# Optimization experiments

Hardware: AMD Instinct MI355X
Metric: run time of the kernel (lower is better)

Reference implementation:

```python
import jax, jax.numpy as jnp
import numpy as np

NUM_GRAPHS = 512
BN_EPS = 1e-5

def _lin(k, fin, fout):
    kw, kb = jax.random.split(k)
    s = 1.0 / np.sqrt(fin)
    return (jax.random.uniform(kw, (fin, fout), jnp.float32, -s, s),
            jax.random.uniform(kb, (fout,), jnp.float32, -s, s))

def setup_inputs() -> dict:
    key = jax.random.key(0)
    ks = jax.random.split(key, 16)
    N, E, F, C, H, O = 50000, 800000, 128, 256, 512, 768
    x = jax.random.normal(ks[0], (N, F), jnp.float32)
    edge_index = jax.random.randint(ks[1], (2, E), 0, N, jnp.int64)
    batch = jnp.sort(jax.random.randint(ks[2], (N,), 0, NUM_GRAPHS, jnp.int64))
    d = {"x": x, "edge_index": edge_index, "batch": batch}
    d["w1a"], d["b1a"] = _lin(ks[3], F, C)
    d["g1"], d["be1"] = jnp.ones((C,), jnp.float32), jnp.zeros((C,), jnp.float32)
    d["w1b"], d["b1b"] = _lin(ks[4], C, C)
    d["w2a"], d["b2a"] = _lin(ks[5], C, C)
    d["g2"], d["be2"] = jnp.ones((C,), jnp.float32), jnp.zeros((C,), jnp.float32)
    d["w2b"], d["b2b"] = _lin(ks[6], C, C)
    d["w3a"], d["b3a"] = _lin(ks[7], C, C)
    d["g3"], d["be3"] = jnp.ones((C,), jnp.float32), jnp.zeros((C,), jnp.float32)
    d["w3b"], d["b3b"] = _lin(ks[8], C, C)
    d["wh1"], d["bh1"] = _lin(ks[9], C, H)
    d["wh2"], d["bh2"] = _lin(ks[10], H, O)
    return d

def _bn(z, g, b):
    mu = jnp.mean(z, axis=0)
    var = jnp.mean((z - mu) ** 2, axis=0)  # biased var, torch BN training mode
    return (z - mu) * jax.lax.rsqrt(var + BN_EPS) * g + b

def _gin(x, edge_index, wa, ba, g, be, wb, bb, tanh_out):
    src, dst = edge_index[0], edge_index[1]
    agg = jax.ops.segment_sum(x[src], dst, num_segments=x.shape[0])
    h = x + agg  # eps = 0
    z = jax.nn.relu(_bn(h @ wa + ba, g, be))
    z = z @ wb + bb
    return jnp.tanh(z) if tanh_out else z

def reference(x, edge_index, batch,
              w1a, b1a, g1, be1, w1b, b1b,
              w2a, b2a, g2, be2, w2b, b2b,
              w3a, b3a, g3, be3, w3b, b3b,
              wh1, bh1, wh2, bh2):
    h = jax.nn.relu(_gin(x, edge_index, w1a, b1a, g1, be1, w1b, b1b, False))
    h = jax.nn.relu(_gin(h, edge_index, w2a, b2a, g2, be2, w2b, b2b, True))
    h = _gin(h, edge_index, w3a, b3a, g3, be3, w3b, b3b, True)
    # global mean pool over graphs
    sums = jax.ops.segment_sum(h, batch, num_segments=NUM_GRAPHS)
    cnt = jax.ops.segment_sum(jnp.ones((h.shape[0],), h.dtype), batch, num_segments=NUM_GRAPHS)
    pooled = sums / jnp.maximum(cnt, 1.0)[:, None]
    z = jax.nn.relu(pooled @ wh1 + bh1)
    return z @ wh2 + bh2
```

## Files before the change

kernel.cpp:

```cpp
#include <hip/hip_runtime.h>


typedef __attribute__((ext_vector_type(8))) short short8;
typedef __attribute__((ext_vector_type(4))) float f32x4;
typedef __attribute__((ext_vector_type(4))) unsigned short us4;
typedef __attribute__((ext_vector_type(8))) unsigned short us8;

__device__ __forceinline__ unsigned short f2bf(float f) {
  unsigned int b = __float_as_uint(f);
  unsigned int r = 0x7FFFu + ((b >> 16) & 1u);
  return (unsigned short)((b + r) >> 16);
}
__device__ __forceinline__ float bf2f(unsigned short u) {
  return __uint_as_float(((unsigned int)u) << 16);
}

__device__ __forceinline__ int sw8(int row) {
  return (row & 7) ^ ((row >> 3) & 7);
}

typedef const __attribute__((address_space(1))) unsigned int* gas1;
typedef __attribute__((address_space(3))) unsigned int* las3;
__device__ __forceinline__ void gload16(const void* g, void* l) {
  __builtin_amdgcn_global_load_lds((gas1)g, (las3)l, 16, 0, 0);
}

__device__ __forceinline__ size_t swz8_idx(int row, int k, int K) {
  int g = k >> 3;
  return (size_t)row * K + ((g >> 3) << 6) + ((((g & 7) ^ sw8(row)) << 3)) + (k & 7);
}

__global__ void k_histbounds(const int* __restrict__ ei, int* __restrict__ deg, int E,
                             int eb, const int* __restrict__ batch,
                             int* __restrict__ gs, int* __restrict__ ge, int N) {
  int b = blockIdx.x;
  if (b < eb) {
    int e = b * 256 + threadIdx.x;
    if (e < E) atomicAdd(&deg[ei[E + e]], 1);
  } else {
    int i = (b - eb) * 256 + threadIdx.x;
    if (i < N) {
      int bb = batch[i];
      if (i == 0 || batch[i - 1] != bb) gs[bb] = i;
      if (i == N - 1 || batch[i + 1] != bb) ge[bb] = i + 1;
    }
  }
}

__global__ __launch_bounds__(1024) void k_scan1(const int* __restrict__ deg,
                                                int* __restrict__ partial,
                                                int* __restrict__ bsum, int N) {
  __shared__ int sd[1024];
  int tid = threadIdx.x;
  int i = blockIdx.x * 1024 + tid;
  int v = (i < N) ? deg[i] : 0;
  sd[tid] = v;
  __syncthreads();
  for (int off = 1; off < 1024; off <<= 1) {
    int t = (tid >= off) ? sd[tid - off] : 0;
    __syncthreads();
    sd[tid] += t;
    __syncthreads();
  }
  if (i < N) partial[i] = sd[tid];
  if (tid == 1023) bsum[blockIdx.x] = sd[1023];
}

__global__ void k_scan2(int* __restrict__ bsum, int nb) {
  int l = threadIdx.x;
  int orig = (l < nb) ? bsum[l] : 0;
  int v = orig;
  for (int off = 1; off < 64; off <<= 1) {
    int t = __shfl_up(v, off);
    if (l >= off) v += t;
  }
  if (l < nb) bsum[l] = v - orig;
}

__global__ void k_scan3(const int* __restrict__ deg, const int* __restrict__ partial,
                        const int* __restrict__ bsum, int* __restrict__ rowptr,
                        int* __restrict__ cursor, int N) {
  int i = blockIdx.x * 256 + threadIdx.x;
  if (i >= N) return;
  int incl = partial[i] + bsum[i >> 10];
  rowptr[i + 1] = incl;
  cursor[i] = incl - deg[i];
  if (i == 0) rowptr[0] = 0;
}

__global__ void k_fill(const int* __restrict__ ei, int* __restrict__ cursor,
                       int* __restrict__ adj, int E) {
  int e = blockIdx.x * 256 + threadIdx.x;
  if (e >= E) return;
  int s = ei[e];
  int d = ei[E + e];
  int pos = atomicAdd(&cursor[d], 1);
  adj[pos] = s;
}

__global__ void k_xbf(const float* __restrict__ X, unsigned short* __restrict__ Xb,
                      int total) {
  int t = blockIdx.x * 256 + threadIdx.x;
  if (t * 8 >= total) return;
  const float4 v0 = *(const float4*)(X + t * 8);
  const float4 v1 = *(const float4*)(X + t * 8 + 4);
  us8 o;
  o[0] = f2bf(v0.x); o[1] = f2bf(v0.y); o[2] = f2bf(v0.z); o[3] = f2bf(v0.w);
  o[4] = f2bf(v1.x); o[5] = f2bf(v1.y); o[6] = f2bf(v1.z); o[7] = f2bf(v1.w);
  *(us8*)(Xb + t * 8) = o;
}

__global__ void k_prep_all(const float* __restrict__ w1a, const float* __restrict__ w1b,
                           const float* __restrict__ w2a, const float* __restrict__ w2b,
                           const float* __restrict__ w3a, const float* __restrict__ w3b,
                           const float* __restrict__ wh1, const float* __restrict__ wh2,
                           unsigned short* __restrict__ Hi, unsigned short* __restrict__ Lo) {
  int idx = blockIdx.x * 256 + threadIdx.x;
  const float* W; int K, Nout, lo_;
  if (idx < 32768)       { W = w1a; K = 128; Nout = 256; lo_ = 0; }
  else if (idx < 98304)  { W = w1b; K = 256; Nout = 256; lo_ = 32768; }
  else if (idx < 163840) { W = w2a; K = 256; Nout = 256; lo_ = 98304; }
  else if (idx < 229376) { W = w2b; K = 256; Nout = 256; lo_ = 163840; }
  else if (idx < 294912) { W = w3a; K = 256; Nout = 256; lo_ = 229376; }
  else if (idx < 360448) { W = w3b; K = 256; Nout = 256; lo_ = 294912; }
  else if (idx < 491520) { W = wh1; K = 256; Nout = 512; lo_ = 360448; }
  else                   { W = wh2; K = 512; Nout = 768; lo_ = 491520; }
  int li = idx - lo_;
  int n = li % Nout, k = li / Nout;
  float w = W[k * Nout + n];
  unsigned short h = f2bf(w);
  size_t oi = (size_t)lo_ + swz8_idx(n, k, K);
  Hi[oi] = h;
  Lo[oi] = f2bf(w - bf2f(h));
}

template <int C>
__global__ __launch_bounds__(256) void k_agg(const unsigned short* __restrict__ Xb,
                                             unsigned short* __restrict__ Hb,
                                             const int* __restrict__ rowptr,
                                             const int* __restrict__ adj, int N,
                                             float* __restrict__ statsZ) {
  if (blockIdx.x == 0) {
    statsZ[threadIdx.x] = 0.f;
    statsZ[256 + threadIdx.x] = 0.f;
  }
  int node = blockIdx.x * 4 + (threadIdx.x >> 6);
  if (node >= N) return;
  int lane = threadIdx.x & 63;
  int e0 = rowptr[node], e1 = rowptr[node + 1];
  if constexpr (C == 256) {
    us4 ov = *(const us4*)(Xb + (size_t)node * C + lane * 4);
    float a0 = bf2f(ov[0]), a1 = bf2f(ov[1]), a2 = bf2f(ov[2]), a3 = bf2f(ov[3]);
    int e = e0;
    for (; e + 4 <= e1; e += 4) {
      int s0 = adj[e], s1 = adj[e + 1], s2 = adj[e + 2], s3 = adj[e + 3];
      us4 v0 = *(const us4*)(Xb + (size_t)s0 * C + lane * 4);
      us4 v1 = *(const us4*)(Xb + (size_t)s1 * C + lane * 4);
      us4 v2 = *(const us4*)(Xb + (size_t)s2 * C + lane * 4);
      us4 v3 = *(const us4*)(Xb + (size_t)s3 * C + lane * 4);
      a0 += (bf2f(v0[0]) + bf2f(v1[0])) + (bf2f(v2[0]) + bf2f(v3[0]));
      a1 += (bf2f(v0[1]) + bf2f(v1[1])) + (bf2f(v2[1]) + bf2f(v3[1]));
      a2 += (bf2f(v0[2]) + bf2f(v1[2])) + (bf2f(v2[2]) + bf2f(v3[2]));
      a3 += (bf2f(v0[3]) + bf2f(v1[3])) + (bf2f(v2[3]) + bf2f(v3[3]));
    }
    for (; e < e1; ++e) {
      us4 v = *(const us4*)(Xb + (size_t)adj[e] * C + lane * 4);
      a0 += bf2f(v[0]); a1 += bf2f(v[1]); a2 += bf2f(v[2]); a3 += bf2f(v[3]);
    }
    us4 hv;
    hv[0] = f2bf(a0); hv[1] = f2bf(a1); hv[2] = f2bf(a2); hv[3] = f2bf(a3);
    size_t oi = (size_t)node * 256 + ((lane >> 4) << 6) +
                ((((lane >> 1) & 7) ^ sw8(node)) << 3) + ((lane & 1) << 2);
    *(us4*)(Hb + oi) = hv;
  } else {
    ushort2 ov = *(const ushort2*)(Xb + (size_t)node * C + lane * 2);
    float a0 = bf2f(ov.x), a1 = bf2f(ov.y);
    int e = e0;
    for (; e + 4 <= e1; e += 4) {
      int s0 = adj[e], s1 = adj[e + 1], s2 = adj[e + 2], s3 = adj[e + 3];
      ushort2 v0 = *(const ushort2*)(Xb + (size_t)s0 * C + lane * 2);
      ushort2 v1 = *(const ushort2*)(Xb + (size_t)s1 * C + lane * 2);
      ushort2 v2 = *(const ushort2*)(Xb + (size_t)s2 * C + lane * 2);
      ushort2 v3 = *(const ushort2*)(Xb + (size_t)s3 * C + lane * 2);
      a0 += (bf2f(v0.x) + bf2f(v1.x)) + (bf2f(v2.x) + bf2f(v3.x));
      a1 += (bf2f(v0.y) + bf2f(v1.y)) + (bf2f(v2.y) + bf2f(v3.y));
    }
    for (; e < e1; ++e) {
      ushort2 v = *(const ushort2*)(Xb + (size_t)adj[e] * C + lane * 2);
      a0 += bf2f(v.x); a1 += bf2f(v.y);
    }
    ushort2 hv = {f2bf(a0), f2bf(a1)};
    size_t oi = (size_t)node * 128 + ((lane >> 5) << 6) +
                ((((lane >> 2) & 7) ^ sw8(node)) << 3) + ((lane & 3) << 1);
    *(ushort2*)(Hb + oi) = hv;
  }
}

template <int EPI, bool STATS, bool OSPLIT, bool XSWZ, int ASRC, bool FULL, bool OBF16>
__global__ __launch_bounds__(256) void k_gemm(
    const unsigned short* __restrict__ AHb, const unsigned short* __restrict__ ALo,
    const unsigned short* __restrict__ Zb,
    int M, int K, int Nld, int mb, int per,
    const unsigned short* __restrict__ WHi, const unsigned short* __restrict__ WLo,
    const float* __restrict__ bias,
    const float* __restrict__ statsIn, const float* __restrict__ gvec,
    const float* __restrict__ bevec,
    float* __restrict__ Out, unsigned short* __restrict__ OutB,
    unsigned short* __restrict__ OHi, unsigned short* __restrict__ OLo,
    float* __restrict__ statsOut) {
  __shared__ unsigned short aHi[4096], bHi[8192];
  __shared__ unsigned short aLo[FULL ? 4096 : 64], bLo[FULL ? 8192 : 64];
  __shared__ float sBNsc[ASRC == 2 ? 256 : 1], sBNsh[ASRC == 2 ? 256 : 1];
  int bx, by;
  if constexpr (XSWZ) {
    int xcd = blockIdx.x & 7, slot = blockIdx.x >> 3;
    bx = xcd * per + (slot >> 1);
    by = slot & 1;
    if (bx >= mb) return;
  } else {
    bx = blockIdx.x;
    by = blockIdx.y;
  }
  const int tid = threadIdx.x;
  const int lane = tid & 63, w = tid >> 6;
  const int wm = w >> 1, wn = w & 1;
  const int m0 = bx * 64, n0 = by * 128;

  if constexpr (ASRC == 2) {
    float mu = statsIn[tid] / (float)M;
    float var = statsIn[256 + tid] / (float)M - mu * mu;
    float sc = gvec[tid] * rsqrtf(var + 1e-5f);
    sBNsc[tid] = sc;
    sBNsh[tid] = bevec[tid] - mu * sc;
    __syncthreads();
  }

  f32x4 zero = {0.f, 0.f, 0.f, 0.f};
  f32x4 acc[2][4];
#pragma unroll
  for (int i = 0; i < 2; ++i)
#pragma unroll
    for (int j = 0; j < 4; ++j) acc[i][j] = zero;

  const int l8 = lane >> 3;
  const int s8 = lane & 7;

  us8 arg[2], brg[4];
  const unsigned short* aptr[2];
  const unsigned short* bptr[4];
  if constexpr (!FULL) {
    const unsigned short* asrc = (ASRC == 2) ? Zb : AHb;
#pragma unroll
    for (int p = 0; p < 2; ++p) {
      int row = (p << 5) + (tid >> 3);
      int ra = m0 + row; if (ra >= M) ra = M - 1;
      aptr[p] = asrc + (size_t)ra * K + (tid & 7) * 8;
      arg[p] = *(const us8*)(aptr[p]);
    }
#pragma unroll
    for (int q = 0; q < 4; ++q) {
      int row = (q << 5) + (tid >> 3);
      bptr[q] = WHi + (size_t)(n0 + row) * K + (tid & 7) * 8;
      brg[q] = *(const us8*)(bptr[q]);
    }
  }

  for (int kb = 0; kb < K; kb += 64) {
    if constexpr (!FULL) {
      if constexpr (ASRC == 2) {
#pragma unroll
        for (int p = 0; p < 2; ++p) {
          int row = (p << 5) + (tid >> 3), gq = tid & 7;
          us8 hv;
#pragma unroll
          for (int jj = 0; jj < 8; ++jj) {
            int kc = kb + gq * 8 + jj;
            float o = fmaxf(bf2f(arg[p][jj]) * sBNsc[kc] + sBNsh[kc], 0.f);
            hv[jj] = f2bf(o);
          }
          int bo = row * 128 + ((gq ^ sw8(row)) << 4);
          *(us8*)((char*)aHi + bo) = hv;
        }
      } else {
#pragma unroll
        for (int p = 0; p < 2; ++p) {
          int row = (p << 5) + (tid >> 3);
          int bo = row * 128 + ((tid & 7) << 4);
          *(us8*)((char*)aHi + bo) = arg[p];
        }
      }
#pragma unroll
      for (int q = 0; q < 4; ++q) {
        int row = (q << 5) + (tid >> 3);
        int bo = row * 128 + ((tid & 7) << 4);
        *(us8*)((char*)bHi + bo) = brg[q];
      }
      __syncthreads();
      if (kb + 64 < K) {
#pragma unroll
        for (int p = 0; p < 2; ++p) arg[p] = *(const us8*)(aptr[p] + kb + 64);
#pragma unroll
        for (int q = 0; q < 4; ++q) brg[q] = *(const us8*)(bptr[q] + kb + 64);
      }
    } else {
      __syncthreads();
#pragma unroll
      for (int q = 0; q < 2; ++q) {
        int row = (w << 4) + (q << 3) + l8;
        int ra = m0 + row; if (ra >= M) ra = M - 1;
        size_t ga = (size_t)ra * K + kb + s8 * 8;
        unsigned boA = (w << 11) + (q << 10);
        gload16(AHb + ga, (char*)aHi + boA);
        gload16(ALo + ga, (char*)aLo + boA);
      }
#pragma unroll
      for (int q = 0; q < 4; ++q) {
        int row = (w << 5) + (q << 3) + l8;
        size_t gb = (size_t)(n0 + row) * K + kb + s8 * 8;
        unsigned bo2 = (w << 12) + (q << 10);
        gload16(WHi + gb, (char*)bHi + bo2);
        gload16(WLo + gb, (char*)bLo + bo2);
      }
      __syncthreads();
    }

    const int j = lane >> 4;
#pragma unroll
    for (int kk = 0; kk < 2; ++kk) {
      int g = (kk << 2) + j;
      short8 bh[4], bl[4];
#pragma unroll
      for (int ni = 0; ni < 4; ++ni) {
        int r = wn * 64 + ni * 16 + (lane & 15);
        int bo = r * 128 + ((g ^ sw8(r)) << 4);
        bh[ni] = *(const short8*)((const char*)bHi + bo);
        if constexpr (FULL) bl[ni] = *(const short8*)((const char*)bLo + bo);
      }
#pragma unroll
      for (int mi = 0; mi < 2; ++mi) {
        int r = wm * 32 + mi * 16 + (lane & 15);
        int bo = r * 128 + ((g ^ sw8(r)) << 4);
        short8 ah = *(const short8*)((const char*)aHi + bo);
#pragma unroll
        for (int ni = 0; ni < 4; ++ni) {
          acc[mi][ni] = __builtin_amdgcn_mfma_f32_16x16x32_bf16(ah, bh[ni], acc[mi][ni], 0, 0, 0);
          if constexpr (FULL) {
            short8 al = *(const short8*)((const char*)aLo + bo);
            acc[mi][ni] = __builtin_amdgcn_mfma_f32_16x16x32_bf16(ah, bl[ni], acc[mi][ni], 0, 0, 0);
            acc[mi][ni] = __builtin_amdgcn_mfma_f32_16x16x32_bf16(al, bh[ni], acc[mi][ni], 0, 0, 0);
          }
        }
      }
    }
    if constexpr (!FULL) __syncthreads();
  }

#pragma unroll
  for (int ni = 0; ni < 4; ++ni) {
    int col = n0 + wn * 64 + ni * 16 + (lane & 15);
    float bc = bias[col];
    float s = 0.f, q = 0.f;
#pragma unroll
    for (int mi = 0; mi < 2; ++mi) {
      int rbase = m0 + wm * 32 + mi * 16 + (lane >> 4) * 4;
#pragma unroll
      for (int r = 0; r < 4; ++r) {
        int row = rbase + r;
        if (row < M) {
          float o = acc[mi][ni][r] + bc;
          if (STATS) { s += o; q += o * o; }
          if (OSPLIT) {
            o = fmaxf(o, 0.f);
            unsigned short h = f2bf(o);
            size_t oi = swz8_idx(row, col, Nld);
            OHi[oi] = h;
            OLo[oi] = f2bf(o - bf2f(h));
          } else {
            if (EPI == 1) o = fmaxf(o, 0.f);
            else if (EPI == 2) o = tanhf(o);
            else if (EPI == 3) o = fmaxf(tanhf(o), 0.f);
            if (OBF16) OutB[(size_t)row * Nld + col] = f2bf(o);
            else       Out[(size_t)row * Nld + col] = o;
          }
        }
      }
    }
    if (STATS) {
      s += __shfl_xor(s, 16); s += __shfl_xor(s, 32);
      q += __shfl_xor(q, 16); q += __shfl_xor(q, 32);
      if ((lane >> 4) == 0) {
        atomicAdd(&statsOut[col], s);
        atomicAdd(&statsOut[256 + col], q);
      }
    }
  }
}

__global__ __launch_bounds__(256) void k_pool(const unsigned short* __restrict__ Hb,
                                              const int* __restrict__ gs,
                                              const int* __restrict__ ge,
                                              unsigned short* __restrict__ PHi,
                                              unsigned short* __restrict__ PLo) {
  __shared__ float4 red[4][64];
  int gi = blockIdx.x;
  int s = gs[gi], e = ge[gi];
  int w = threadIdx.x >> 6, lane = threadIdx.x & 63;
  float4 acc = {0.f, 0.f, 0.f, 0.f};
  for (int r = s + w; r < e; r += 4) {
    us4 v = *(const us4*)(Hb + (size_t)r * 256 + lane * 4);
    acc.x += bf2f(v[0]); acc.y += bf2f(v[1]);
    acc.z += bf2f(v[2]); acc.w += bf2f(v[3]);
  }
  red[w][lane] = acc;
  __syncthreads();
  if (w == 0) {
    float4 a = red[0][lane], b = red[1][lane], c = red[2][lane], d = red[3][lane];
    float inv = 1.0f / fmaxf((float)(e - s), 1.0f);
    float vv[4] = {(a.x + b.x + c.x + d.x) * inv, (a.y + b.y + c.y + d.y) * inv,
                   (a.z + b.z + c.z + d.z) * inv, (a.w + b.w + c.w + d.w) * inv};
    us4 hv, lv;
#pragma unroll
    for (int j = 0; j < 4; ++j) {
      unsigned short h = f2bf(vv[j]);
      hv[j] = h;
      lv[j] = f2bf(vv[j] - bf2f(h));
    }
    size_t oi = (size_t)gi * 256 + ((lane >> 4) << 6) +
                ((((lane >> 1) & 7) ^ sw8(gi)) << 3) + ((lane & 1) << 2);
    *(us4*)(PHi + oi) = hv;
    *(us4*)(PLo + oi) = lv;
  }
}

extern "C" void kernel_launch(void* const* d_in, const int* in_sizes, int n_in,
                              void* d_out, int out_size, void* d_ws, size_t ws_size,
                              hipStream_t stream) {
  const float* x      = (const float*)d_in[0];
  const int* ei       = (const int*)d_in[1];
  const int* bat      = (const int*)d_in[2];
  const float* w1a = (const float*)d_in[3];  const float* b1a = (const float*)d_in[4];
  const float* g1  = (const float*)d_in[5];  const float* be1 = (const float*)d_in[6];
  const float* w1b = (const float*)d_in[7];  const float* b1b = (const float*)d_in[8];
  const float* w2a = (const float*)d_in[9];  const float* b2a = (const float*)d_in[10];
  const float* g2  = (const float*)d_in[11]; const float* be2 = (const float*)d_in[12];
  const float* w2b = (const float*)d_in[13]; const float* b2b = (const float*)d_in[14];
  const float* w3a = (const float*)d_in[15]; const float* b3a = (const float*)d_in[16];
  const float* g3  = (const float*)d_in[17]; const float* be3 = (const float*)d_in[18];
  const float* w3b = (const float*)d_in[19]; const float* b3b = (const float*)d_in[20];
  const float* wh1 = (const float*)d_in[21]; const float* bh1 = (const float*)d_in[22];
  const float* wh2 = (const float*)d_in[23]; const float* bh2 = (const float*)d_in[24];
  float* out = (float*)d_out;

  const int N = in_sizes[0] / 128;
  const int E = in_sizes[1] / 2;
  const int G = 512;

  char* ws = (char*)d_ws;
  size_t off = 0;
  auto alloc = [&](size_t bytes) {
    void* p = ws + off;
    off = (off + bytes + 255) & ~(size_t)255;
    return p;
  };
  unsigned short* hb = (unsigned short*)alloc((size_t)N * 256 * 2);
  unsigned short* zb = (unsigned short*)alloc((size_t)N * 256 * 2);
  unsigned short* ab = (unsigned short*)alloc((size_t)N * 256 * 2);
  unsigned short* xb = (unsigned short*)alloc((size_t)N * 128 * 2);
  int* adj     = (int*)alloc((size_t)E * 4);
  int* rowptr  = (int*)alloc((size_t)(N + 1) * 4);
  int* cursor  = (int*)alloc((size_t)N * 4);
  int* deg     = (int*)alloc((size_t)N * 4);
  int* partial = (int*)alloc((size_t)N * 4);
  int* bsum    = (int*)alloc(64 * 4);
  unsigned short* wHi = (unsigned short*)alloc(884736 * 2);
  unsigned short* wLo = (unsigned short*)alloc(884736 * 2);
  float* stats = (float*)alloc(512 * 4);
  int* gs      = (int*)alloc(G * 4);
  int* ge      = (int*)alloc(G * 4);
  unsigned short* poolHi = (unsigned short*)alloc((size_t)G * 256 * 2);
  unsigned short* poolLo = (unsigned short*)alloc((size_t)G * 256 * 2);
  unsigned short* thidHi = (unsigned short*)alloc((size_t)G * 512 * 2);
  unsigned short* thidLo = (unsigned short*)alloc((size_t)G * 512 * 2);

  const int o1a = 0, o1b = 32768, o2a = 98304, o2b = 163840, o3a = 229376, o3b = 294912;
  const int oh1 = 360448, oh2 = 491520;

  hipMemsetAsync(deg, 0, (size_t)N * 4, stream);
  hipMemsetAsync(gs, 0, (size_t)G * 4, stream);
  hipMemsetAsync(ge, 0, (size_t)G * 4, stream);

  int eb = (E + 255) / 256;
  int nbN = (N + 255) / 256;
  int nb1 = (N + 1023) >> 10;
  k_histbounds<<<eb + nbN, 256, 0, stream>>>(ei, deg, E, eb, bat, gs, ge, N);
  k_scan1<<<nb1, 1024, 0, stream>>>(deg, partial, bsum, N);
  k_scan2<<<1, 64, 0, stream>>>(bsum, nb1);
  k_scan3<<<nbN, 256, 0, stream>>>(deg, partial, bsum, rowptr, cursor, N);
  k_fill<<<eb, 256, 0, stream>>>(ei, cursor, adj, E);

  k_xbf<<<(N * 128 / 8 + 255) / 256, 256, 0, stream>>>(x, xb, N * 128);
  k_prep_all<<<3456, 256, 0, stream>>>(w1a, w1b, w2a, w2b, w3a, w3b, wh1, wh2, wHi, wLo);

  int nb4 = (N + 3) / 4;
  const int mb = (N + 63) / 64;
  const int per = (mb + 7) / 8;
  dim3 gg(per * 16);

  k_agg<128><<<nb4, 256, 0, stream>>>(xb, hb, rowptr, adj, N, stats);
  k_gemm<0, true, false, true, 0, false, true><<<gg, 256, 0, stream>>>(
      hb, nullptr, nullptr, N, 128, 256, mb, per, wHi + o1a, wLo + o1a, b1a,
      nullptr, nullptr, nullptr, nullptr, zb, nullptr, nullptr, stats);
  k_gemm<1, false, false, true, 2, false, true><<<gg, 256, 0, stream>>>(
      nullptr, nullptr, zb, N, 256, 256, mb, per, wHi + o1b, wLo + o1b, b1b,
      stats, g1, be1, nullptr, ab, nullptr, nullptr, nullptr);

  k_agg<256><<<nb4, 256, 0, stream>>>(ab, hb, rowptr, adj, N, stats);
  k_gemm<0, true, false, true, 0, false, true><<<gg, 256, 0, stream>>>(
      hb, nullptr, nullptr, N, 256, 256, mb, per, wHi + o2a, wLo + o2a, b2a,
      nullptr, nullptr, nullptr, nullptr, zb, nullptr, nullptr, stats);
  k_gemm<3, false, false, true, 2, false, true><<<gg, 256, 0, stream>>>(
      nullptr, nullptr, zb, N, 256, 256, mb, per, wHi + o2b, wLo + o2b, b2b,
      stats, g2, be2, nullptr, ab, nullptr, nullptr, nullptr);

  k_agg<256><<<nb4, 256, 0, stream>>>(ab, hb, rowptr, adj, N, stats);
  k_gemm<0, true, false, true, 0, false, true><<<gg, 256, 0, stream>>>(
      hb, nullptr, nullptr, N, 256, 256, mb, per, wHi + o3a, wLo + o3a, b3a,
      nullptr, nullptr, nullptr, nullptr, zb, nullptr, nullptr, stats);
  k_gemm<2, false, false, true, 2, false, true><<<gg, 256, 0, stream>>>(
      nullptr, nullptr, zb, N, 256, 256, mb, per, wHi + o3b, wLo + o3b, b3b,
      stats, g3, be3, nullptr, ab, nullptr, nullptr, nullptr);

  k_pool<<<G, 256, 0, stream>>>(ab, gs, ge, poolHi, poolLo);
  dim3 gh1(8, 4);
  k_gemm<1, false, true, false, 0, true, false><<<gh1, 256, 0, stream>>>(
      poolHi, poolLo, nullptr, G, 256, 512, 0, 0, wHi + oh1, wLo + oh1, bh1,
      nullptr, nullptr, nullptr, nullptr, nullptr, thidHi, thidLo, nullptr);
  dim3 gh2(8, 6);
  k_gemm<0, false, false, false, 0, true, false><<<gh2, 256, 0, stream>>>(
      thidHi, thidLo, nullptr, G, 512, 768, 0, 0, wHi + oh2, wLo + oh2, bh2,
      nullptr, nullptr, nullptr, out, nullptr, nullptr, nullptr, nullptr);
}
```

Baseline: 577.3 us.

## Use persistent node GEMM keeping full weight slice in LDS, A read directly to registers

Splits the generic GEMM into a persistent node-layer kernel and a head kernel. The node-layer kernel loads its whole 128-column weight slice into LDS once, then loops over several 64-row tiles. For each tile it reads the A rows straight from global memory into MFMA fragment registers, which removes the per-K-step LDS staging and barriers for A. The aggregation output is written unswizzled to match the new row-major A reads. This trades barrier and LDS traffic for a larger LDS footprint (up to 64KB), which may lower occupancy, and for uncoalesced fragment-pattern global loads.

Result: slower. 700.1 us (+21.3%).

```diff
diff --git a/kernel.cpp b/kernel.cpp
--- a/kernel.cpp
+++ b/kernel.cpp
@@ -169,9 +169,7 @@
     }
     us4 hv;
     hv[0] = f2bf(a0); hv[1] = f2bf(a1); hv[2] = f2bf(a2); hv[3] = f2bf(a3);
-    size_t oi = (size_t)node * 256 + ((lane >> 4) << 6) +
-                ((((lane >> 1) & 7) ^ sw8(node)) << 3) + ((lane & 1) << 2);
-    *(us4*)(Hb + oi) = hv;
+    *(us4*)(Hb + (size_t)node * C + lane * 4) = hv;
   } else {
     ushort2 ov = *(const ushort2*)(Xb + (size_t)node * C + lane * 2);
     float a0 = bf2f(ov.x), a1 = bf2f(ov.y);
@@ -190,41 +188,31 @@
       a0 += bf2f(v.x); a1 += bf2f(v.y);
     }
     ushort2 hv = {f2bf(a0), f2bf(a1)};
-    size_t oi = (size_t)node * 128 + ((lane >> 5) << 6) +
-                ((((lane >> 2) & 7) ^ sw8(node)) << 3) + ((lane & 3) << 1);
-    *(ushort2*)(Hb + oi) = hv;
-  }
-}
-
-template <int EPI, bool STATS, bool OSPLIT, bool XSWZ, int ASRC, bool FULL, bool OBF16>
-__global__ __launch_bounds__(256) void k_gemm(
-    const unsigned short* __restrict__ AHb, const unsigned short* __restrict__ ALo,
-    const unsigned short* __restrict__ Zb,
-    int M, int K, int Nld, int mb, int per,
-    const unsigned short* __restrict__ WHi, const unsigned short* __restrict__ WLo,
+    *(ushort2*)(Hb + (size_t)node * C + lane * 2) = hv;
+  }
+}
+
+template <int EPI, bool STATS, int ASRC, int KT>
+__global__ __launch_bounds__(256) void k_gemmM(
+    const unsigned short* __restrict__ Ab, int M,
+    const unsigned short* __restrict__ WHi,
     const float* __restrict__ bias,
     const float* __restrict__ statsIn, const float* __restrict__ gvec,
     const float* __restrict__ bevec,
-    float* __restrict__ Out, unsigned short* __restrict__ OutB,
-    unsigned short* __restrict__ OHi, unsigned short* __restrict__ OLo,
-    float* __restrict__ statsOut) {
-  __shared__ unsigned short aHi[4096], bHi[8192];
-  __shared__ unsigned short aLo[FULL ? 4096 : 64], bLo[FULL ? 8192 : 64];
+    unsigned short* __restrict__ OutB,
+    float* __restrict__ statsOut,
+    int mb, int per) {
+  constexpr int SLOTS = KT / 8;
+  constexpr int KS = KT / 32;
+  __shared__ unsigned short bB[128 * KT];
   __shared__ float sBNsc[ASRC == 2 ? 256 : 1], sBNsh[ASRC == 2 ? 256 : 1];
-  int bx, by;
-  if constexpr (XSWZ) {
-    int xcd = blockIdx.x & 7, slot = blockIdx.x >> 3;
-    bx = xcd * per + (slot >> 1);
-    by = slot & 1;
-    if (bx >= mb) return;
-  } else {
-    bx = blockIdx.x;
-    by = blockIdx.y;
-  }
+
   const int tid = threadIdx.x;
   const int lane = tid & 63, w = tid >> 6;
   const int wm = w >> 1, wn = w & 1;
-  const int m0 = bx * 64, n0 = by * 128;
+  const int xcd = blockIdx.x & 7, slot = blockIdx.x >> 3;
+  const int by = slot & 1, bseq = slot >> 1;
+  const int n0 = by * 128;
 
   if constexpr (ASRC == 2) {
     float mu = statsIn[tid] / (float)M;
@@ -232,8 +220,126 @@
     float sc = gvec[tid] * rsqrtf(var + 1e-5f);
     sBNsc[tid] = sc;
     sBNsh[tid] = bevec[tid] - mu * sc;
-    __syncthreads();
-  }
+  }
+
+  constexpr int ROUNDS = (128 * SLOTS) / 256;
+#pragma unroll
+  for (int q = 0; q < ROUNDS; ++q) {
+    int cb = q * 256 + w * 64;
+    int c = cb + lane;
+    int row = c / SLOTS, sl = c % SLOTS;
+    size_t gb = (size_t)(n0 + row) * KT + sl * 8;
+    gload16(WHi + gb, (char*)bB + cb * 16);
+  }
+  __syncthreads();
+
+  const int fr = lane & 15;
+  const int j4 = lane >> 4;
+  const int fk = j4 * 8;
+
+  for (int i = 0;; ++i) {
+    int bxl = bseq + i * 32;
+    if (bxl >= per) break;
+    int bx = xcd * per + bxl;
+    if (bx >= mb) break;
+    int m0 = bx * 64;
+
+    us8 av[2][KS];
+#pragma unroll
+    for (int mi = 0; mi < 2; ++mi) {
+      int ra = m0 + wm * 32 + mi * 16 + fr;
+      if (ra >= M) ra = M - 1;
+      const unsigned short* ap = Ab + (size_t)ra * KT + fk;
+#pragma unroll
+      for (int ks = 0; ks < KS; ++ks) av[mi][ks] = *(const us8*)(ap + ks * 32);
+    }
+    if constexpr (ASRC == 2) {
+#pragma unroll
+      for (int mi = 0; mi < 2; ++mi)
+#pragma unroll
+        for (int ks = 0; ks < KS; ++ks) {
+#pragma unroll
+          for (int jj = 0; jj < 8; ++jj) {
+            int kc = ks * 32 + fk + jj;
+            float o = fmaxf(bf2f(av[mi][ks][jj]) * sBNsc[kc] + sBNsh[kc], 0.f);
+            av[mi][ks][jj] = f2bf(o);
+          }
+        }
+    }
+
+    f32x4 acc[2][4];
+    f32x4 zero = {0.f, 0.f, 0.f, 0.f};
+#pragma unroll
+    for (int a = 0; a < 2; ++a)
+#pragma unroll
+      for (int b = 0; b < 4; ++b) acc[a][b] = zero;
+
+#pragma unroll
+    for (int ks = 0; ks < KS; ++ks) {
+      int g = ks * 4 + j4;
+      short8 bh[4];
+#pragma unroll
+      for (int ni = 0; ni < 4; ++ni) {
+        int r = wn * 64 + ni * 16 + fr;
+        int bo = r * (KT * 2) + ((g >> 3) << 7) + (((g & 7) ^ sw8(r)) << 4);
+        bh[ni] = *(const short8*)((const char*)bB + bo);
+      }
+#pragma unroll
+      for (int mi = 0; mi < 2; ++mi)
+#pragma unroll
+        for (int ni = 0; ni < 4; ++ni)
+          acc[mi][ni] = __builtin_amdgcn_mfma_f32_16x16x32_bf16(
+              (short8)av[mi][ks], bh[ni], acc[mi][ni], 0, 0, 0);
+    }
+
+#pragma unroll
+    for (int ni = 0; ni < 4; ++ni) {
+      int col = n0 + wn * 64 + ni * 16 + fr;
+      float bc = bias[col];
+      float s = 0.f, qq = 0.f;
+#pragma unroll
+      for (int mi = 0; mi < 2; ++mi) {
+        int rbase = m0 + wm * 32 + mi * 16 + (lane >> 4) * 4;
+#pragma unroll
+        for (int r = 0; r < 4; ++r) {
+          int row = rbase + r;
+          if (row < M) {
+            float o = acc[mi][ni][r] + bc;
+            if (STATS) { s += o; qq += o * o; }
+            if (EPI == 1) o = fmaxf(o, 0.f);
+            else if (EPI == 2) o = tanhf(o);
+            else if (EPI == 3) o = fmaxf(tanhf(o), 0.f);
+            OutB[(size_t)row * 256 + col] = f2bf(o);
+          }
+        }
+      }
+      if (STATS) {
+        s += __shfl_xor(s, 16); s += __shfl_xor(s, 32);
+        qq += __shfl_xor(qq, 16); qq += __shfl_xor(qq, 32);
+        if ((lane >> 4) == 0) {
+          atomicAdd(&statsOut[col], s);
+          atomicAdd(&statsOut[256 + col], qq);
+        }
+      }
+    }
+  }
+}
+
+template <int EPI, bool OSPLIT>
+__global__ __launch_bounds__(256) void k_gemmH(
+    const unsigned short* __restrict__ AHb, const unsigned short* __restrict__ ALo,
+    int M, int K, int Nld,
+    const unsigned short* __restrict__ WHi, const unsigned short* __restrict__ WLo,
+    const float* __restrict__ bias,
+    float* __restrict__ Out,
+    unsigned short* __restrict__ OHi, unsigned short* __restrict__ OLo) {
+  __shared__ unsigned short aHi[4096], bHi[8192];
+  __shared__ unsigned short aLo[4096], bLo[8192];
+  int bx = blockIdx.x, by = blockIdx.y;
+  const int tid = threadIdx.x;
+  const int lane = tid & 63, w = tid >> 6;
+  const int wm = w >> 1, wn = w & 1;
+  const int m0 = bx * 64, n0 = by * 128;
 
   f32x4 zero = {0.f, 0.f, 0.f, 0.f};
   f32x4 acc[2][4];
@@ -245,84 +351,26 @@
   const int l8 = lane >> 3;
   const int s8 = lane & 7;
 
-  us8 arg[2], brg[4];
-  const unsigned short* aptr[2];
-  const unsigned short* bptr[4];
-  if constexpr (!FULL) {
-    const unsigned short* asrc = (ASRC == 2) ? Zb : AHb;
-#pragma unroll
-    for (int p = 0; p < 2; ++p) {
-      int row = (p << 5) + (tid >> 3);
+  for (int kb = 0; kb < K; kb += 64) {
+    __syncthreads();
+#pragma unroll
+    for (int q = 0; q < 2; ++q) {
+      int row = (w << 4) + (q << 3) + l8;
       int ra = m0 + row; if (ra >= M) ra = M - 1;
-      aptr[p] = asrc + (size_t)ra * K + (tid & 7) * 8;
-      arg[p] = *(const us8*)(aptr[p]);
+      size_t ga = (size_t)ra * K + kb + s8 * 8;
+      unsigned boA = (w << 11) + (q << 10);
+      gload16(AHb + ga, (char*)aHi + boA);
+      gload16(ALo + ga, (char*)aLo + boA);
     }
 #pragma unroll
     for (int q = 0; q < 4; ++q) {
-      int row = (q << 5) + (tid >> 3);
-      bptr[q] = WHi + (size_t)(n0 + row) * K + (tid & 7) * 8;
-      brg[q] = *(const us8*)(bptr[q]);
-    }
-  }
-
-  for (int kb = 0; kb < K; kb += 64) {
-    if constexpr (!FULL) {
-      if constexpr (ASRC == 2) {
-#pragma unroll
-        for (int p = 0; p < 2; ++p) {
-          int row = (p << 5) + (tid >> 3), gq = tid & 7;
-          us8 hv;
-#pragma unroll
-          for (int jj = 0; jj < 8; ++jj) {
-            int kc = kb + gq * 8 + jj;
-            float o = fmaxf(bf2f(arg[p][jj]) * sBNsc[kc] + sBNsh[kc], 0.f);
-            hv[jj] = f2bf(o);
-          }
-          int bo = row * 128 + ((gq ^ sw8(row)) << 4);
-          *(us8*)((char*)aHi + bo) = hv;
-        }
-      } else {
-#pragma unroll
-        for (int p = 0; p < 2; ++p) {
-          int row = (p << 5) + (tid >> 3);
-          int bo = row * 128 + ((tid & 7) << 4);
-          *(us8*)((char*)aHi + bo) = arg[p];
-        }
-      }
-#pragma unroll
-      for (int q = 0; q < 4; ++q) {
-        int row = (q << 5) + (tid >> 3);
-        int bo = row * 128 + ((tid & 7) << 4);
-        *(us8*)((char*)bHi + bo) = brg[q];
-      }
-      __syncthreads();
-      if (kb + 64 < K) {
-#pragma unroll
-        for (int p = 0; p < 2; ++p) arg[p] = *(const us8*)(aptr[p] + kb + 64);
-#pragma unroll
-        for (int q = 0; q < 4; ++q) brg[q] = *(const us8*)(bptr[q] + kb + 64);
-      }
-    } else {
-      __syncthreads();
-#pragma unroll
-      for (int q = 0; q < 2; ++q) {
-        int row = (w << 4) + (q << 3) + l8;
-        int ra = m0 + row; if (ra >= M) ra = M - 1;
-        size_t ga = (size_t)ra * K + kb + s8 * 8;
-        unsigned boA = (w << 11) + (q << 10);
-        gload16(AHb + ga, (char*)aHi + boA);
-        gload16(ALo + ga, (char*)aLo + boA);
-      }
-#pragma unroll
-      for (int q = 0; q < 4; ++q) {
-        int row = (w << 5) + (q << 3) + l8;
-        size_t gb = (size_t)(n0 + row) * K + kb + s8 * 8;
-        unsigned bo2 = (w << 12) + (q << 10);
-        gload16(WHi + gb, (char*)bHi + bo2);
-        gload16(WLo + gb, (char*)bLo + bo2);
-      }
-      __syncthreads();
-    }
+      int row = (w << 5) + (q << 3) + l8;
+      size_t gb = (size_t)(n0 + row) * K + kb + s8 * 8;
+      unsigned bo2 = (w << 12) + (q << 10);
+      gload16(WHi + gb, (char*)bHi + bo2);
+      gload16(WLo + gb, (char*)bLo + bo2);
+    }
+    __syncthreads();
 
     const int j = lane >> 4;
 #pragma unroll
@@ -334,32 +382,28 @@
         int r = wn * 64 + ni * 16 + (lane & 15);
         int bo = r * 128 + ((g ^ sw8(r)) << 4);
         bh[ni] = *(const short8*)((const char*)bHi + bo);
-        if constexpr (FULL) bl[ni] = *(const short8*)((const char*)bLo + bo);
+        bl[ni] = *(const short8*)((const char*)bLo + bo);
       }
 #pragma unroll
       for (int mi = 0; mi < 2; ++mi) {
         int r = wm * 32 + mi * 16 + (lane & 15);
         int bo = r * 128 + ((g ^ sw8(r)) << 4);
         short8 ah = *(const short8*)((const char*)aHi + bo);
+        short8 al = *(const short8*)((const char*)aLo + bo);
 #pragma unroll
         for (int ni = 0; ni < 4; ++ni) {
           acc[mi][ni] = __builtin_amdgcn_mfma_f32_16x16x32_bf16(ah, bh[ni], acc[mi][ni], 0, 0, 0);
-          if constexpr (FULL) {
-            short8 al = *(const short8*)((const char*)aLo + bo);
-            acc[mi][ni] = __builtin_amdgcn_mfma_f32_16x16x32_bf16(ah, bl[ni], acc[mi][ni], 0, 0, 0);
-            acc[mi][ni] = __builtin_amdgcn_mfma_f32_16x16x32_bf16(al, bh[ni], acc[mi][ni], 0, 0, 0);
-          }
+          acc[mi][ni] = __builtin_amdgcn_mfma_f32_16x16x32_bf16(ah, bl[ni], acc[mi][ni], 0, 0, 0);
+          acc[mi][ni] = __builtin_amdgcn_mfma_f32_16x16x32_bf16(al, bh[ni], acc[mi][ni], 0, 0, 0);
         }
       }
     }
-    if constexpr (!FULL) __syncthreads();
   }
 
 #pragma unroll
   for (int ni = 0; ni < 4; ++ni) {
     int col = n0 + wn * 64 + ni * 16 + (lane & 15);
     float bc = bias[col];
-    float s = 0.f, q = 0.f;
 #pragma unroll
     for (int mi = 0; mi < 2; ++mi) {
       int rbase = m0 + wm * 32 + mi * 16 + (lane >> 4) * 4;
@@ -368,7 +412,6 @@
         int row = rbase + r;
         if (row < M) {
           float o = acc[mi][ni][r] + bc;
-          if (STATS) { s += o; q += o * o; }
           if (OSPLIT) {
             o = fmaxf(o, 0.f);
             unsigned short h = f2bf(o);
@@ -377,20 +420,9 @@
             OLo[oi] = f2bf(o - bf2f(h));
           } else {
             if (EPI == 1) o = fmaxf(o, 0.f);
-            else if (EPI == 2) o = tanhf(o);
-            else if (EPI == 3) o = fmaxf(tanhf(o), 0.f);
-            if (OBF16) OutB[(size_t)row * Nld + col] = f2bf(o);
-            else       Out[(size_t)row * Nld + col] = o;
+            Out[(size_t)row * Nld + col] = o;
           }
         }
-      }
-    }
-    if (STATS) {
-      s += __shfl_xor(s, 16); s += __shfl_xor(s, 32);
-      q += __shfl_xor(q, 16); q += __shfl_xor(q, 32);
-      if ((lane >> 4) == 0) {
-        atomicAdd(&statsOut[col], s);
-        atomicAdd(&statsOut[256 + col], q);
       }
     }
   }
@@ -504,39 +536,33 @@
   int nb4 = (N + 3) / 4;
   const int mb = (N + 63) / 64;
   const int per = (mb + 7) / 8;
-  dim3 gg(per * 16);
+  dim3 gm(512);
 
   k_agg<128><<<nb4, 256, 0, stream>>>(xb, hb, rowptr, adj, N, stats);
-  k_gemm<0, true, false, true, 0, false, true><<<gg, 256, 0, stream>>>(
-      hb, nullptr, nullptr, N, 128, 256, mb, per, wHi + o1a, wLo + o1a, b1a,
-      nullptr, nullptr, nullptr, nullptr, zb, nullptr, nullptr, stats);
-  k_gemm<1, false, false, true, 2, false, true><<<gg, 256, 0, stream>>>(
-      nullptr, nullptr, zb, N, 256, 256, mb, per, wHi + o1b, wLo + o1b, b1b,
-      stats, g1, be1, nullptr, ab, nullptr, nullptr, nullptr);
+  k_gemmM<0, true, 0, 128><<<gm, 256, 0, stream>>>(
+      hb, N, wHi + o1a, b1a, nullptr, nullptr, nullptr, zb, stats, mb, per);
+  k_gemmM<1, false, 2, 256><<<gm, 256, 0, stream>>>(
+      zb, N, wHi + o1b, b1b, stats, g1, be1, ab, nullptr, mb, per);
 
   k_agg<256><<<nb4, 256, 0, stream>>>(ab, hb, rowptr, adj, N, stats);
-  k_gemm<0, true, false, true, 0, false, true><<<gg, 256, 0, stream>>>(
-      hb, nullptr, nullptr, N, 256, 256, mb, per, wHi + o2a, wLo + o2a, b2a,
-      nullptr, nullptr, nullptr, nullptr, zb, nullptr, nullptr, stats);
-  k_gemm<3, false, false, true, 2, false, true><<<gg, 256, 0, stream>>>(
-      nullptr, nullptr, zb, N, 256, 256, mb, per, wHi + o2b, wLo + o2b, b2b,
-      stats, g2, be2, nullptr, ab, nullptr, nullptr, nullptr);
+  k_gemmM<0, true, 0, 256><<<gm, 256, 0, stream>>>(
+      hb, N, wHi + o2a, b2a, nullptr, nullptr, nullptr, zb, stats, mb, per);
+  k_gemmM<3, false, 2, 256><<<gm, 256, 0, stream>>>(
+      zb, N, wHi + o2b, b2b, stats, g2, be2, ab, nullptr, mb, per);
 
   k_agg<256><<<nb4, 256, 0, stream>>>(ab, hb, rowptr, adj, N, stats);
-  k_gemm<0, true, false, true, 0, false, true><<<gg, 256, 0, stream>>>(
-      hb, nullptr, nullptr, N, 256, 256, mb, per, wHi + o3a, wLo + o3a, b3a,
-      nullptr, nullptr, nullptr, nullptr, zb, nullptr, nullptr, stats);
-  k_gemm<2, false, false, true, 2, false, true><<<gg, 256, 0, stream>>>(
-      nullptr, nullptr, zb, N, 256, 256, mb, per, wHi + o3b, wLo + o3b, b3b,
-      stats, g3, be3, nullptr, ab, nullptr, nullptr, nullptr);
+  k_gemmM<0, true, 0, 256><<<gm, 256, 0, stream>>>(
+      hb, N, wHi + o3a, b3a, nullptr, nullptr, nullptr, zb, stats, mb, per);
+  k_gemmM<2, false, 2, 256><<<gm, 256, 0, stream>>>(
+      zb, N, wHi + o3b, b3b, stats, g3, be3, ab, nullptr, mb, per);
 
   k_pool<<<G, 256, 0, stream>>>(ab, gs, ge, poolHi, poolLo);
   dim3 gh1(8, 4);
-  k_gemm<1, false, true, false, 0, true, false><<<gh1, 256, 0, stream>>>(
-      poolHi, poolLo, nullptr, G, 256, 512, 0, 0, wHi + oh1, wLo + oh1, bh1,
-      nullptr, nullptr, nullptr, nullptr, nullptr, thidHi, thidLo, nullptr);
+  k_gemmH<1, true><<<gh1, 256, 0, stream>>>(
+      poolHi, poolLo, G, 256, 512, wHi + oh1, wLo + oh1, bh1,
+      nullptr, thidHi, thidLo);
   dim3 gh2(8, 6);
-  k_gemm<0, false, false, false, 0, true, false><<<gh2, 256, 0, stream>>>(
-      thidHi, thidLo, nullptr, G, 512, 768, 0, 0, wHi + oh2, wLo + oh2, bh2,
-      nullptr, nullptr, nullptr, out, nullptr, nullptr, nullptr, nullptr);
-}
+  k_gemmH<0, false><<<gh2, 256, 0, stream>>>(
+      thidHi, thidLo, G, 512, 768, wHi + oh2, wLo + oh2, bh2,
+      out, nullptr, nullptr);
+}
```
